# Kernel tuning notes

Hardware: AMD Instinct MI355X
Metric: run time of the kernel (lower is better)

The kernel has to match this reference:

```python
import jax, jax.numpy as jnp
import numpy as np

B, H, S, D, HID = 2, 4, 512, 16, 32

def setup_inputs() -> dict:
    key = jax.random.key(0)
    ks = jax.random.split(key, 12)
    sc = 1.0 / np.sqrt(D)
    return {
        "v": jax.random.normal(ks[0], (B, H, S, D), jnp.float32),
        "k": jax.random.normal(ks[1], (B, H, S, D), jnp.float32),
        "q": jax.random.normal(ks[2], (B, H, S, D), jnp.float32),
        "mask": jnp.zeros((B, 1, S, S), jnp.float32),
        "Wq": jax.random.normal(ks[3], (D, D), jnp.float32) * sc,
        "bq": jnp.zeros((D,), jnp.float32),
        "Wk": jax.random.normal(ks[4], (D, D), jnp.float32) * sc,
        "bk": jnp.zeros((D,), jnp.float32),
        "Wv": jax.random.normal(ks[5], (D, D), jnp.float32) * sc,
        "bv": jnp.zeros((D,), jnp.float32),
        "Wo": jax.random.normal(ks[6], (D, D), jnp.float32) * sc,
        "bo": jnp.zeros((D,), jnp.float32),
        "N1": jax.random.normal(ks[7], (2 * D, HID), jnp.float32) * (1.0 / np.sqrt(2 * D)),
        "b1": jnp.zeros((HID,), jnp.float32),
        "N2": jax.random.normal(ks[8], (HID, 1), jnp.float32) * (1.0 / np.sqrt(HID)),
        "b2": jnp.zeros((1,), jnp.float32),
    }

def _pair_mlp_scores(qh, kh, N1, b1, N2, b2):
    # NN(concat(q_i, k_j)) computed without materializing the 2*D concat:
    # first layer = q_i @ N1[:D] + k_j @ N1[D:] + b1, broadcast-summed over pairs.
    d = qh.shape[-1]
    A, Bm = N1[:d], N1[d:]
    hq = jnp.einsum("bhsd,df->bhsf", qh, A)   # (B,H,Sq,HID)
    hk = jnp.einsum("bhsd,df->bhsf", kh, Bm)  # (B,H,Sk,HID)
    pre = hq[:, :, :, None, :] + hk[:, :, None, :, :] + b1  # (B,H,Sq,Sk,HID)
    return jnp.einsum("bhqkf,fo->bhqk", jax.nn.relu(pre), N2[:, :]) + b2[0]

def reference(v, k, q, mask, Wq, bq, Wk, bk, Wv, bv, Wo, bo, N1, b1, N2, b2):
    qp = q @ Wq + bq
    kp = k @ Wk + bk
    vp = v @ Wv + bv
    logits = _pair_mlp_scores(qp, kp, N1, b1, N2, b2)
    # make_sym=True: add NN(concat(k_j, q_i))
    logits = logits + _pair_mlp_scores(kp, qp, N1, b1, N2, b2).swapaxes(-1, -2)
    logits = logits + mask * -1e9
    attn = jax.nn.softmax(logits, axis=-1)          # (B,H,Sq,Sk)
    out = jnp.einsum("bhqk,bhkd->bhqd", attn, vp)   # (B,H,Sq,D)
    return out @ Wo + bo, attn
```

## Files before the change

kernel.cpp:

```cpp
#include <hip/hip_runtime.h>

#define NB 2
#define NH 4
#define NS 512
#define ND 16
#define NF 32

__global__ __launch_bounds__(256) void k_proj(
    const float* __restrict__ q, const float* __restrict__ kin, const float* __restrict__ v,
    const float* __restrict__ Wq, const float* __restrict__ bq,
    const float* __restrict__ Wk, const float* __restrict__ bk,
    const float* __restrict__ Wv, const float* __restrict__ bv,
    const float* __restrict__ N1, const float* __restrict__ b1,
    float* __restrict__ hq, float* __restrict__ hk, float* __restrict__ vpt)
{
    __shared__ float m_s[16 * 32];
    __shared__ float c_s[32];

    const int bid = blockIdx.x;
    const int job = bid % 5;
    const int sc  = (bid / 5) & 1;
    const int bh  = bid / 10;
    const int t   = threadIdx.x;

    const float* W    = (job < 2) ? Wq : (job < 4 ? Wk : Wv);
    const float* bias = (job < 2) ? bq : (job < 4 ? bk : bv);
    const float* x    = (job < 2) ? q  : (job < 4 ? kin : v);

    if (job < 4) {
        const int noff = (job & 1) * 16;
        for (int i = t; i < 512; i += 256) {
            int e = i >> 5, f = i & 31;
            float m = 0.f;
#pragma unroll
            for (int d = 0; d < 16; ++d)
                m = fmaf(W[e * 16 + d], N1[(noff + d) * 32 + f], m);
            m_s[i] = m;
        }
        if (t < 32) {
            float c = (job & 1) ? b1[t] : 0.f;
#pragma unroll
            for (int d = 0; d < 16; ++d)
                c = fmaf(bias[d], N1[(noff + d) * 32 + t], c);
            c_s[t] = c;
        }
    } else {
        int e = t >> 4, d = t & 15;
        m_s[e * 32 + d] = W[e * 16 + d];
        if (t < 16) c_s[t] = bias[t];
    }
    __syncthreads();

    const int s = sc * 256 + t;
    const int r = bh * NS + s;

    float xv[16];
    const float4* x4 = (const float4*)(x + (size_t)r * 16);
#pragma unroll
    for (int j = 0; j < 4; ++j) {
        float4 a = x4[j];
        xv[4*j] = a.x; xv[4*j+1] = a.y; xv[4*j+2] = a.z; xv[4*j+3] = a.w;
    }

    if (job < 4) {
        float* outb = ((job < 2) ? hq : hk) + (size_t)bh * 32768 + (size_t)(job & 1) * 16384;
        float h[32];
#pragma unroll
        for (int f = 0; f < 32; ++f) h[f] = c_s[f];
#pragma unroll
        for (int e = 0; e < 16; ++e)
#pragma unroll
            for (int f = 0; f < 32; ++f)
                h[f] = fmaf(xv[e], m_s[e * 32 + f], h[f]);
#pragma unroll
        for (int f = 0; f < 32; ++f)
            outb[(size_t)f * NS + s] = h[f];
    } else {
        float* outb = vpt + (size_t)bh * 8192;
        float h[16];
#pragma unroll
        for (int d = 0; d < 16; ++d) h[d] = c_s[d];
#pragma unroll
        for (int e = 0; e < 16; ++e)
#pragma unroll
            for (int d = 0; d < 16; ++d)
                h[d] = fmaf(xv[e], m_s[e * 32 + d], h[d]);
#pragma unroll
        for (int d = 0; d < 16; ++d)
            outb[(size_t)d * NS + s] = h[d];
    }
}

__global__ __launch_bounds__(512) void k_fused(
    const float* __restrict__ hq, const float* __restrict__ hk,
    const float* __restrict__ vpt,
    const float* __restrict__ N2, const float* __restrict__ b2,
    const float* __restrict__ mask,
    const float* __restrict__ Wo, const float* __restrict__ bo,
    float* __restrict__ attn, float* __restrict__ out)
{
    __shared__ __align__(16) float hq_s[16 * 68];
    __shared__ __align__(16) float attn_s[16 * 516];
    __shared__ float wo_s[256];
    __shared__ float bo_s[16];
    __shared__ float ov_s[256];
    __shared__ float part_s[2304];
    __shared__ float redm[128];
    __shared__ float reds[128];

    const int bh  = blockIdx.x >> 5;
    const int q0  = (blockIdx.x & 31) << 4;
    const int tid = threadIdx.x;
    const int wave = tid >> 6, lane = tid & 63;
    const int k = tid;
    const size_t base = (size_t)bh * 32768;

    float hkA_l[32], hkB_l[32], n2_l[32], mreg[16];
#pragma unroll
    for (int f = 0; f < 32; ++f) hkA_l[f] = hk[base + (size_t)f * NS + k];
#pragma unroll
    for (int f = 0; f < 32; ++f) hkB_l[f] = hk[base + (size_t)(32+f) * NS + k];
#pragma unroll
    for (int f = 0; f < 32; ++f) n2_l[f] = N2[f];
    const int b = bh >> 2;
    const float* mbase = mask + (size_t)b * NS * NS;
#pragma unroll
    for (int qi = 0; qi < 16; ++qi) mreg[qi] = mbase[(size_t)(q0 + qi) * NS + k];
    const float b2v = 2.0f * b2[0];

    for (int i = tid; i < 1024; i += 512) {
        int f = i >> 4, qi = i & 15;
        hq_s[qi * 68 + f] = hq[base + (size_t)f * NS + q0 + qi];
    }
    if (tid < 256) wo_s[tid] = Wo[tid];
    if (tid < 16)  bo_s[tid] = bo[tid];
    __syncthreads();

    float sreg[16];
#pragma unroll
    for (int qi = 0; qi < 16; ++qi) {
        const float4* hq4 = (const float4*)&hq_s[qi * 68];
        float s0 = b2v, s1 = 0.f, s2 = 0.f, s3 = 0.f;
#pragma unroll
        for (int f4 = 0; f4 < 8; ++f4) {
            float4 ha = hq4[f4];
            float4 hb = hq4[8 + f4];
            {
                const int f = 4*f4;
                float a = fmaxf(ha.x + hkB_l[f], 0.f) + fmaxf(hb.x + hkA_l[f], 0.f);
                s0 = fmaf(n2_l[f], a, s0);
            }
            {
                const int f = 4*f4 + 1;
                float a = fmaxf(ha.y + hkB_l[f], 0.f) + fmaxf(hb.y + hkA_l[f], 0.f);
                s1 = fmaf(n2_l[f], a, s1);
            }
            {
                const int f = 4*f4 + 2;
                float a = fmaxf(ha.z + hkB_l[f], 0.f) + fmaxf(hb.z + hkA_l[f], 0.f);
                s2 = fmaf(n2_l[f], a, s2);
            }
            {
                const int f = 4*f4 + 3;
                float a = fmaxf(ha.w + hkB_l[f], 0.f) + fmaxf(hb.w + hkA_l[f], 0.f);
                s3 = fmaf(n2_l[f], a, s3);
            }
        }
        float s = (s0 + s1) + (s2 + s3);
        s = fmaf(mreg[qi], -1e9f, s);
        sreg[qi] = s;

        float m = s;
#pragma unroll
        for (int off = 32; off > 0; off >>= 1) m = fmaxf(m, __shfl_xor(m, off));
        if (lane == 0) redm[qi * 8 + wave] = m;
    }
    __syncthreads();

    float preg[16];
#pragma unroll
    for (int qi = 0; qi < 16; ++qi) {
        float bm = redm[qi * 8];
#pragma unroll
        for (int w = 1; w < 8; ++w) bm = fmaxf(bm, redm[qi * 8 + w]);
        float e = __expf(sreg[qi] - bm);
        preg[qi] = e;
        float ss = e;
#pragma unroll
        for (int off = 32; off > 0; off >>= 1) ss += __shfl_xor(ss, off);
        if (lane == 0) reds[qi * 8 + wave] = ss;
    }
    __syncthreads();

#pragma unroll
    for (int qi = 0; qi < 16; ++qi) {
        float tot = reds[qi * 8];
#pragma unroll
        for (int w = 1; w < 8; ++w) tot += reds[qi * 8 + w];
        float p = preg[qi] / tot;
        attn[(size_t)(bh * NS + q0 + qi) * NS + k] = p;
        attn_s[qi * 516 + k] = p;
    }
    __syncthreads();

    {
        const int qi_p  = tid & 15;
        const int dgrp  = (tid >> 4) & 3;
        const int khalf = tid >> 6;
        const float4* a4 = (const float4*)attn_s;
        const float4* v4 = (const float4*)(vpt + (size_t)bh * 8192);
        float acc0 = 0.f, acc1 = 0.f, acc2 = 0.f, acc3 = 0.f;
#pragma unroll
        for (int kq = 0; kq < 16; ++kq) {
            const int k4 = khalf * 16 + kq;
            float4 av = a4[qi_p * 129 + k4];
            float4 w0 = v4[(dgrp * 4 + 0) * 128 + k4];
            float4 w1 = v4[(dgrp * 4 + 1) * 128 + k4];
            float4 w2 = v4[(dgrp * 4 + 2) * 128 + k4];
            float4 w3 = v4[(dgrp * 4 + 3) * 128 + k4];
            acc0 = fmaf(av.x, w0.x, fmaf(av.y, w0.y, fmaf(av.z, w0.z, fmaf(av.w, w0.w, acc0))));
            acc1 = fmaf(av.x, w1.x, fmaf(av.y, w1.y, fmaf(av.z, w1.z, fmaf(av.w, w1.w, acc1))));
            acc2 = fmaf(av.x, w2.x, fmaf(av.y, w2.y, fmaf(av.z, w2.z, fmaf(av.w, w2.w, acc2))));
            acc3 = fmaf(av.x, w3.x, fmaf(av.y, w3.y, fmaf(av.z, w3.z, fmaf(av.w, w3.w, acc3))));
        }
        part_s[(qi_p * 16 + dgrp * 4 + 0) * 9 + khalf] = acc0;
        part_s[(qi_p * 16 + dgrp * 4 + 1) * 9 + khalf] = acc1;
        part_s[(qi_p * 16 + dgrp * 4 + 2) * 9 + khalf] = acc2;
        part_s[(qi_p * 16 + dgrp * 4 + 3) * 9 + khalf] = acc3;
    }
    __syncthreads();

    if (tid < 256) {
        const int qi2 = tid >> 4, d = tid & 15;
        float ov = 0.f;
#pragma unroll
        for (int kh = 0; kh < 8; ++kh) ov += part_s[(qi2 * 16 + d) * 9 + kh];
        ov_s[qi2 * 16 + d] = ov;
    }
    __syncthreads();

    if (tid < 256) {
        const int qi2 = tid >> 4, d = tid & 15;
        float res = bo_s[d];
#pragma unroll
        for (int e = 0; e < 16; ++e)
            res = fmaf(ov_s[qi2 * 16 + e], wo_s[e * 16 + d], res);
        out[(size_t)(bh * NS + q0 + qi2) * 16 + d] = res;
    }
}

extern "C" void kernel_launch(void* const* d_in, const int* in_sizes, int n_in,
                              void* d_out, int out_size, void* d_ws, size_t ws_size,
                              hipStream_t stream)
{
    const float* v    = (const float*)d_in[0];
    const float* k    = (const float*)d_in[1];
    const float* q    = (const float*)d_in[2];
    const float* mask = (const float*)d_in[3];
    const float* Wq   = (const float*)d_in[4];
    const float* bq   = (const float*)d_in[5];
    const float* Wk   = (const float*)d_in[6];
    const float* bk   = (const float*)d_in[7];
    const float* Wv   = (const float*)d_in[8];
    const float* bv   = (const float*)d_in[9];
    const float* Wo   = (const float*)d_in[10];
    const float* bo   = (const float*)d_in[11];
    const float* N1   = (const float*)d_in[12];
    const float* b1   = (const float*)d_in[13];
    const float* N2   = (const float*)d_in[14];
    const float* b2   = (const float*)d_in[15];

    float* out  = (float*)d_out;
    float* attn = out + (size_t)NB*NH*NS*ND;

    float* hq  = (float*)d_ws;
    float* hk  = hq + (size_t)8 * 32768;
    float* vpt = hk + (size_t)8 * 32768;

    k_proj <<<80, 256, 0, stream>>>(q, k, v, Wq, bq, Wk, bk, Wv, bv, N1, b1, hq, hk, vpt);
    k_fused<<<256, 512, 0, stream>>>(hq, hk, vpt, N2, b2, mask, Wo, bo, attn, out);
}
```

Measured before the change: 38.07 us.

## Halve query rows per block, use packed v2f math, and raise occupancy

Each block of the fused score kernel now handles 8 query rows instead of 16, which doubles the grid to 512 blocks and adds a min-blocks-per-CU launch bound to cut register pressure. The pair-MLP inner loop uses 2-wide float vectors so the compiler can emit packed FP32 ops. Mask values are prefetched one row ahead instead of held in registers, and exp is recomputed rather than stored. The attn·V reduction layout is adjusted to the smaller tile. The cost is that each block reloads the 64 hk features per key for half as many rows, and exp is computed twice.

```diff
diff --git a/kernel.cpp b/kernel.cpp
--- a/kernel.cpp
+++ b/kernel.cpp
@@ -5,6 +5,9 @@
 #define NS 512
 #define ND 16
 #define NF 32
+
+typedef float v2f __attribute__((ext_vector_type(2)));
+
 
 __global__ __launch_bounds__(256) void k_proj(
     const float* __restrict__ q, const float* __restrict__ kin, const float* __restrict__ v,
@@ -91,7 +94,7 @@
     }
 }
 
-__global__ __launch_bounds__(512) void k_fused(
+__global__ __launch_bounds__(512, 4) void k_fused(
     const float* __restrict__ hq, const float* __restrict__ hk,
     const float* __restrict__ vpt,
     const float* __restrict__ N2, const float* __restrict__ b2,
@@ -99,75 +102,62 @@
     const float* __restrict__ Wo, const float* __restrict__ bo,
     float* __restrict__ attn, float* __restrict__ out)
 {
-    __shared__ __align__(16) float hq_s[16 * 68];
-    __shared__ __align__(16) float attn_s[16 * 516];
+    __shared__ __align__(16) float hq_s[8 * 68];
+    __shared__ __align__(16) float attn_s[8 * 516];
     __shared__ float wo_s[256];
     __shared__ float bo_s[16];
-    __shared__ float ov_s[256];
-    __shared__ float part_s[2304];
-    __shared__ float redm[128];
-    __shared__ float reds[128];
-
-    const int bh  = blockIdx.x >> 5;
-    const int q0  = (blockIdx.x & 31) << 4;
+    __shared__ float ov_s[128];
+    __shared__ float part_s[128 * 17];
+    __shared__ float redm[64];
+    __shared__ float reds[64];
+
+    const int bh  = blockIdx.x >> 6;
+    const int q0  = (blockIdx.x & 63) << 3;
     const int tid = threadIdx.x;
     const int wave = tid >> 6, lane = tid & 63;
     const int k = tid;
     const size_t base = (size_t)bh * 32768;
 
-    float hkA_l[32], hkB_l[32], n2_l[32], mreg[16];
-#pragma unroll
-    for (int f = 0; f < 32; ++f) hkA_l[f] = hk[base + (size_t)f * NS + k];
-#pragma unroll
-    for (int f = 0; f < 32; ++f) hkB_l[f] = hk[base + (size_t)(32+f) * NS + k];
-#pragma unroll
-    for (int f = 0; f < 32; ++f) n2_l[f] = N2[f];
-    const int b = bh >> 2;
-    const float* mbase = mask + (size_t)b * NS * NS;
-#pragma unroll
-    for (int qi = 0; qi < 16; ++qi) mreg[qi] = mbase[(size_t)(q0 + qi) * NS + k];
+    v2f hk2A[16], hk2B[16], n2v[16];
+#pragma unroll
+    for (int f2 = 0; f2 < 16; ++f2) {
+        hk2A[f2] = (v2f){ hk[base + (size_t)(2*f2    ) * NS + k],
+                          hk[base + (size_t)(2*f2 + 1) * NS + k] };
+        hk2B[f2] = (v2f){ hk[base + (size_t)(32 + 2*f2) * NS + k],
+                          hk[base + (size_t)(33 + 2*f2) * NS + k] };
+        n2v[f2]  = (v2f){ N2[2*f2], N2[2*f2 + 1] };
+    }
     const float b2v = 2.0f * b2[0];
-
-    for (int i = tid; i < 1024; i += 512) {
-        int f = i >> 4, qi = i & 15;
+    const float* mbase = mask + (size_t)(bh >> 2) * NS * NS;
+
+    {
+        int f = tid >> 3, qi = tid & 7;
         hq_s[qi * 68 + f] = hq[base + (size_t)f * NS + q0 + qi];
     }
     if (tid < 256) wo_s[tid] = Wo[tid];
     if (tid < 16)  bo_s[tid] = bo[tid];
     __syncthreads();
 
-    float sreg[16];
-#pragma unroll
-    for (int qi = 0; qi < 16; ++qi) {
-        const float4* hq4 = (const float4*)&hq_s[qi * 68];
-        float s0 = b2v, s1 = 0.f, s2 = 0.f, s3 = 0.f;
-#pragma unroll
-        for (int f4 = 0; f4 < 8; ++f4) {
-            float4 ha = hq4[f4];
-            float4 hb = hq4[8 + f4];
-            {
-                const int f = 4*f4;
-                float a = fmaxf(ha.x + hkB_l[f], 0.f) + fmaxf(hb.x + hkA_l[f], 0.f);
-                s0 = fmaf(n2_l[f], a, s0);
-            }
-            {
-                const int f = 4*f4 + 1;
-                float a = fmaxf(ha.y + hkB_l[f], 0.f) + fmaxf(hb.y + hkA_l[f], 0.f);
-                s1 = fmaf(n2_l[f], a, s1);
-            }
-            {
-                const int f = 4*f4 + 2;
-                float a = fmaxf(ha.z + hkB_l[f], 0.f) + fmaxf(hb.z + hkA_l[f], 0.f);
-                s2 = fmaf(n2_l[f], a, s2);
-            }
-            {
-                const int f = 4*f4 + 3;
-                float a = fmaxf(ha.w + hkB_l[f], 0.f) + fmaxf(hb.w + hkA_l[f], 0.f);
-                s3 = fmaf(n2_l[f], a, s3);
-            }
-        }
-        float s = (s0 + s1) + (s2 + s3);
-        s = fmaf(mreg[qi], -1e9f, s);
+    float sreg[8];
+    float mnext = mbase[(size_t)q0 * NS + k];
+#pragma unroll
+    for (int qi = 0; qi < 8; ++qi) {
+        float mcur = mnext;
+        if (qi < 7) mnext = mbase[(size_t)(q0 + qi + 1) * NS + k];
+        const v2f* hq2 = (const v2f*)(hq_s + qi * 68);
+        v2f acc_a = 0.f, acc_b = 0.f;
+        const v2f z = 0.f;
+#pragma unroll
+        for (int f2 = 0; f2 < 16; ++f2) {
+            v2f t1 = hq2[f2]      + hk2B[f2];
+            v2f t2 = hq2[16 + f2] + hk2A[f2];
+            v2f r  = __builtin_elementwise_max(t1, z) + __builtin_elementwise_max(t2, z);
+            if (f2 & 1) acc_b += n2v[f2] * r;
+            else        acc_a += n2v[f2] * r;
+        }
+        v2f av = acc_a + acc_b;
+        float s = av.x + av.y + b2v;
+        s = fmaf(mcur, -1e9f, s);
         sreg[qi] = s;
 
         float m = s;
@@ -177,14 +167,14 @@
     }
     __syncthreads();
 
-    float preg[16];
-#pragma unroll
-    for (int qi = 0; qi < 16; ++qi) {
+#pragma unroll
+    for (int qi = 0; qi < 8; ++qi) {
         float bm = redm[qi * 8];
 #pragma unroll
         for (int w = 1; w < 8; ++w) bm = fmaxf(bm, redm[qi * 8 + w]);
-        float e = __expf(sreg[qi] - bm);
-        preg[qi] = e;
+        float sm = sreg[qi] - bm;
+        sreg[qi] = sm;
+        float e = __expf(sm);
         float ss = e;
 #pragma unroll
         for (int off = 32; off > 0; off >>= 1) ss += __shfl_xor(ss, off);
@@ -193,26 +183,26 @@
     __syncthreads();
 
 #pragma unroll
-    for (int qi = 0; qi < 16; ++qi) {
+    for (int qi = 0; qi < 8; ++qi) {
         float tot = reds[qi * 8];
 #pragma unroll
         for (int w = 1; w < 8; ++w) tot += reds[qi * 8 + w];
-        float p = preg[qi] / tot;
+        float p = __expf(sreg[qi]) / tot;
         attn[(size_t)(bh * NS + q0 + qi) * NS + k] = p;
         attn_s[qi * 516 + k] = p;
     }
     __syncthreads();
 
     {
-        const int qi_p  = tid & 15;
-        const int dgrp  = (tid >> 4) & 3;
-        const int khalf = tid >> 6;
+        const int qi_p = tid & 7;
+        const int dgrp = (tid >> 3) & 3;
+        const int koct = tid >> 5;
         const float4* a4 = (const float4*)attn_s;
         const float4* v4 = (const float4*)(vpt + (size_t)bh * 8192);
         float acc0 = 0.f, acc1 = 0.f, acc2 = 0.f, acc3 = 0.f;
 #pragma unroll
-        for (int kq = 0; kq < 16; ++kq) {
-            const int k4 = khalf * 16 + kq;
+        for (int kq = 0; kq < 8; ++kq) {
+            const int k4 = koct * 8 + kq;
             float4 av = a4[qi_p * 129 + k4];
             float4 w0 = v4[(dgrp * 4 + 0) * 128 + k4];
             float4 w1 = v4[(dgrp * 4 + 1) * 128 + k4];
@@ -223,23 +213,22 @@
             acc2 = fmaf(av.x, w2.x, fmaf(av.y, w2.y, fmaf(av.z, w2.z, fmaf(av.w, w2.w, acc2))));
             acc3 = fmaf(av.x, w3.x, fmaf(av.y, w3.y, fmaf(av.z, w3.z, fmaf(av.w, w3.w, acc3))));
         }
-        part_s[(qi_p * 16 + dgrp * 4 + 0) * 9 + khalf] = acc0;
-        part_s[(qi_p * 16 + dgrp * 4 + 1) * 9 + khalf] = acc1;
-        part_s[(qi_p * 16 + dgrp * 4 + 2) * 9 + khalf] = acc2;
-        part_s[(qi_p * 16 + dgrp * 4 + 3) * 9 + khalf] = acc3;
-    }
-    __syncthreads();
-
-    if (tid < 256) {
-        const int qi2 = tid >> 4, d = tid & 15;
+        part_s[(qi_p * 16 + dgrp * 4 + 0) * 17 + koct] = acc0;
+        part_s[(qi_p * 16 + dgrp * 4 + 1) * 17 + koct] = acc1;
+        part_s[(qi_p * 16 + dgrp * 4 + 2) * 17 + koct] = acc2;
+        part_s[(qi_p * 16 + dgrp * 4 + 3) * 17 + koct] = acc3;
+    }
+    __syncthreads();
+
+    if (tid < 128) {
         float ov = 0.f;
 #pragma unroll
-        for (int kh = 0; kh < 8; ++kh) ov += part_s[(qi2 * 16 + d) * 9 + kh];
-        ov_s[qi2 * 16 + d] = ov;
-    }
-    __syncthreads();
-
-    if (tid < 256) {
+        for (int kh = 0; kh < 16; ++kh) ov += part_s[tid * 17 + kh];
+        ov_s[tid] = ov;
+    }
+    __syncthreads();
+
+    if (tid < 128) {
         const int qi2 = tid >> 4, d = tid & 15;
         float res = bo_s[d];
 #pragma unroll
@@ -278,5 +267,5 @@
     float* vpt = hk + (size_t)8 * 32768;
 
     k_proj <<<80, 256, 0, stream>>>(q, k, v, Wq, bq, Wk, bk, Wv, bv, N1, b1, hq, hk, vpt);
-    k_fused<<<256, 512, 0, stream>>>(hq, hk, vpt, N2, b2, mask, Wo, bo, attn, out);
+    k_fused<<<512, 512, 0, stream>>>(hq, hk, vpt, N2, b2, mask, Wo, bo, attn, out);
 }
```

Result: faster. 34.49 us (-9.4%).
